# Kernel tuning notes

Hardware: AMD Instinct MI355X
Metric: run time of the kernel (lower is better)

Reference implementation:

```python
import jax, jax.numpy as jnp
import numpy as np
from jax import lax

B, T, U, V = 4, 200, 100, 1024
D_ENC, D_DEC, J = 144, 320, 320


def setup_inputs() -> dict:
    key = jax.random.key(0)
    ks = jax.random.split(key, 8)
    s = lambda d: 1.0 / np.sqrt(d).astype(np.float32)
    return {
        "enc_out": jax.random.normal(ks[0], (B, T, D_ENC), jnp.float32),
        "dec_out": jax.random.normal(ks[1], (B, U + 1, D_DEC), jnp.float32),
        "W_enc": jax.random.normal(ks[2], (D_ENC, J), jnp.float32) * s(D_ENC),
        "b_enc": jnp.zeros((J,), jnp.float32),
        "W_dec": jax.random.normal(ks[3], (D_DEC, J), jnp.float32) * s(D_DEC),
        "b_dec": jnp.zeros((J,), jnp.float32),
        "W_out": jax.random.normal(ks[4], (J, V), jnp.float32) * s(J),
        "b_out": jnp.zeros((V,), jnp.float32),
        "targets": jax.random.randint(ks[5], (B, U), 1, V, jnp.int32),
        "enc_lengths": jax.random.randint(ks[6], (B,), T // 2, T + 1, jnp.int32),
        "target_lengths": jax.random.randint(ks[7], (B,), U // 2, U + 1, jnp.int32),
    }


def _rnnt_loss(log_probs, targets, enc_lengths, target_lengths):
    # log_probs: [B, T, U+1, V]; blank index = 0 (matches RNNTLoss(blank=0))
    blank_lp = log_probs[..., 0]  # [B, T, U+1]
    idx = jnp.broadcast_to(targets[:, None, :, None].astype(jnp.int32), (B, T, U, 1))
    emit_lp = jnp.take_along_axis(log_probs[:, :, :U, :], idx, axis=-1)[..., 0]  # [B, T, U]

    # alpha[0, u] = sum of emit log-probs along u at t=0
    alpha0 = jnp.concatenate(
        [jnp.zeros((B, 1), log_probs.dtype), jnp.cumsum(emit_lp[:, 0, :], axis=1)], axis=1
    )  # [B, U+1]

    def row(a, emit_t):
        # a: alpha_prev + blank (vertical transitions), [B, U+1]; emit_t: [B, U]
        def step(prev, xs):
            a_u, e_prev = xs
            cur = jnp.logaddexp(a_u, prev + e_prev)
            return cur, cur
        _, rest = lax.scan(step, a[:, 0], (a[:, 1:].T, emit_t.T))  # rest: [U, B]
        return jnp.concatenate([a[:, :1], rest.T], axis=1)

    def t_step(alpha_prev, xs):
        blank_prev, emit_t = xs
        alpha_t = row(alpha_prev + blank_prev, emit_t)
        return alpha_t, alpha_t

    xs = (jnp.swapaxes(blank_lp[:, :-1, :], 0, 1), jnp.swapaxes(emit_lp[:, 1:, :], 0, 1))
    _, alphas_rest = lax.scan(t_step, alpha0, xs)  # [T-1, B, U+1]
    alphas = jnp.concatenate([alpha0[None], alphas_rest], axis=0)  # [T, B, U+1]

    b_idx = jnp.arange(B)
    t_idx = enc_lengths - 1
    ll = alphas[t_idx, b_idx, target_lengths] + blank_lp[b_idx, t_idx, target_lengths]
    return jnp.mean(-ll)  # reduction='mean' over batch


def reference(enc_out, dec_out, W_enc, b_enc, W_dec, b_dec, W_out, b_out, targets, enc_lengths, target_lengths):
    enc_p = enc_out @ W_enc + b_enc  # [B, T, J]
    dec_p = dec_out @ W_dec + b_dec  # [B, U+1, J]
    joint = jnp.tanh(enc_p[:, :, None, :] + dec_p[:, None, :, :])  # [B, T, U+1, J]
    logits = joint @ W_out + b_out  # [B, T, U+1, V]
    log_probs = jax.nn.log_softmax(logits, axis=-1)
    return _rnnt_loss(log_probs, targets, enc_lengths, target_lengths)
```

## Files before the change

kernel.cpp:

```cpp
#include <hip/hip_runtime.h>
#include <hip/hip_bf16.h>
#include <math.h>

#define B_ 4
#define T_ 200
#define U_ 100
#define V_ 1024
#define DE 144
#define DD 320
#define J_ 320
#define M_TOT (B_ * T_ * (U_ + 1))
#define SSTR 328
#define DSTR 104
#define NDIAG 300
#define LOG2E 1.4426950408889634f

typedef __attribute__((ext_vector_type(8))) short bf16x8_t;
typedef __attribute__((ext_vector_type(4))) float f32x4_t;

__device__ __forceinline__ float fast_tanh(float x) {
    float e = exp2f(x * (2.0f * LOG2E));
    float r = __frcp_rn(e + 1.0f);
    return fmaf(-2.0f, r, 1.0f);
}

__device__ __forceinline__ ushort f2bf(float x) {
    uint u = __float_as_uint(x);
    uint r = (u + 0x7FFFu + ((u >> 16) & 1u)) >> 16;
    return (ushort)r;
}

template <int K>
__device__ __forceinline__ void proj_body(const float* __restrict__ X,
                                          const float* __restrict__ W,
                                          const float* __restrict__ bias,
                                          float* __restrict__ Y,
                                          int r0, int R, float* sx, int tid) {
    constexpr int QK = K / 4;
    for (int q = tid; q < 16 * QK; q += 640) {
        int row = q / QK;
        int kq = q - row * QK;
        int r = r0 + row;
        if (r >= R) r = R - 1;
        *(float4*)&sx[row * K + kq * 4] = *(const float4*)&X[r * K + kq * 4];
    }
    __syncthreads();
    const int half = (tid >= 320) ? 1 : 0;
    const int c = tid - half * 320;
    float acc[8];
#pragma unroll
    for (int i = 0; i < 8; i++) acc[i] = 0.0f;
    for (int k = 0; k < K; k += 4) {
        float w0 = W[(k + 0) * 320 + c];
        float w1 = W[(k + 1) * 320 + c];
        float w2 = W[(k + 2) * 320 + c];
        float w3 = W[(k + 3) * 320 + c];
#pragma unroll
        for (int i = 0; i < 8; i++) {
            const float4 x4 = *(const float4*)&sx[(half * 8 + i) * K + k];
            acc[i] = fmaf(x4.x, w0, acc[i]);
            acc[i] = fmaf(x4.y, w1, acc[i]);
            acc[i] = fmaf(x4.z, w2, acc[i]);
            acc[i] = fmaf(x4.w, w3, acc[i]);
        }
    }
    const float bb = bias[c];
#pragma unroll
    for (int i = 0; i < 8; i++) {
        int r = r0 + half * 8 + i;
        if (r < R) Y[r * 320 + c] = acc[i] + bb;
    }
}

__global__ __launch_bounds__(640) void prep_kernel(
    const float* __restrict__ enc_out, const float* __restrict__ dec_out,
    const float* __restrict__ W_enc, const float* __restrict__ b_enc,
    const float* __restrict__ W_dec, const float* __restrict__ b_dec,
    const float* __restrict__ W_out,
    float* __restrict__ enc_p, float* __restrict__ dec_p,
    ushort* __restrict__ Wt) {
    __shared__ float sx[16 * 320];
    const int bid = blockIdx.x;
    const int tid = threadIdx.x;
    if (bid < 50) {
        proj_body<DE>(enc_out, W_enc, b_enc, enc_p, bid * 16, B_ * T_, sx, tid);
    } else if (bid < 76) {
        proj_body<DD>(dec_out, W_dec, b_dec, dec_p, (bid - 50) * 16,
                      B_ * (U_ + 1), sx, tid);
    } else {
        int idx = (bid - 76) * 640 + tid;
        int k = idx >> 10;
        int v = idx & 1023;
        ushort b = f2bf(W_out[idx]);
        int frag = (v >> 4) * 10 + (k >> 5);
        int lane = (v & 15) | (((k >> 3) & 3) << 4);
        int elem = k & 7;
        Wt[frag * 512 + lane * 8 + elem] = b;
    }
}

__global__ __launch_bounds__(1024, 4) void joint_mfma(
    const float* __restrict__ enc_p, const float* __restrict__ dec_p,
    const ushort* __restrict__ Wt, const float* __restrict__ b_out,
    const int* __restrict__ targets,
    float* __restrict__ bsk, float* __restrict__ esk) {
    __shared__ ushort sh[64 * SSTR];
    __shared__ float partm[16][64];
    __shared__ float parts[16][64];
    __shared__ float lse_sh[64];
    __shared__ int tgt_sh[64];

    const int tid = threadIdx.x;
    const int r0 = blockIdx.x * 64;

    if (tid < 64) {
        int rc = r0 + tid;
        int tg = -1;
        if (rc < M_TOT) {
            int b = rc / 20200;
            int rem = rc - b * 20200;
            int u = rem - (rem / 101) * 101;
            if (u < U_) tg = targets[b * U_ + u];
        }
        tgt_sh[tid] = tg;
    }

    {
        const int si = tid >> 4;
        const int sq = tid & 15;
        int rc = r0 + si;
        if (rc > M_TOT - 1) rc = M_TOT - 1;
        int b = rc / 20200;
        int rem = rc - b * 20200;
        int t = rem / 101;
        int u = rem - t * 101;
        const float4* ep = (const float4*)&enc_p[(b * 200 + t) * 320];
        const float4* dp = (const float4*)&dec_p[(b * 101 + u) * 320];
        ushort* shp = &sh[si * SSTR];
#pragma unroll
        for (int it = 0; it < 5; it++) {
            int kq = sq + it * 16;
            float4 e = ep[kq];
            float4 dd = dp[kq];
            float t0 = fast_tanh(e.x + dd.x);
            float t1 = fast_tanh(e.y + dd.y);
            float t2 = fast_tanh(e.z + dd.z);
            float t3 = fast_tanh(e.w + dd.w);
            __hip_bfloat162 p0 = __float22bfloat162_rn(make_float2(t0, t1));
            __hip_bfloat162 p1 = __float22bfloat162_rn(make_float2(t2, t3));
            uint2 pk;
            pk.x = *(uint*)&p0;
            pk.y = *(uint*)&p1;
            *(uint2*)&shp[kq * 4] = pk;
        }
    }
    __syncthreads();

    const int wave = tid >> 6;
    const int lane = tid & 63;
    const int lrow = lane & 15;
    const int lk = (lane >> 4) * 8;
    const int cb16 = wave * 4;

    f32x4_t acc[4][4];
#pragma unroll
    for (int mt = 0; mt < 4; mt++)
#pragma unroll
        for (int nt = 0; nt < 4; nt++) acc[mt][nt] = (f32x4_t)(0.0f);

    for (int ks = 0; ks < 10; ks++) {
        bf16x8_t a[4];
#pragma unroll
        for (int mt = 0; mt < 4; mt++)
            a[mt] = *(const bf16x8_t*)&sh[(mt * 16 + lrow) * SSTR + ks * 32 + lk];
#pragma unroll
        for (int nt = 0; nt < 4; nt++) {
            bf16x8_t bfr = *(const bf16x8_t*)&Wt[(((cb16 + nt) * 10 + ks) << 9) + lane * 8];
            __builtin_amdgcn_s_setprio(1);
#pragma unroll
            for (int mt = 0; mt < 4; mt++)
                acc[mt][nt] = __builtin_amdgcn_mfma_f32_16x16x32_bf16(a[mt], bfr, acc[mt][nt], 0, 0, 0);
            __builtin_amdgcn_s_setprio(0);
        }
    }

    float bo[4];
#pragma unroll
    for (int nt = 0; nt < 4; nt++) bo[nt] = b_out[wave * 64 + nt * 16 + lrow];
#pragma unroll
    for (int mt = 0; mt < 4; mt++)
#pragma unroll
        for (int nt = 0; nt < 4; nt++) acc[mt][nt] += bo[nt];

#pragma unroll
    for (int mt = 0; mt < 4; mt++) {
#pragma unroll
        for (int j = 0; j < 4; j++) {
            float m = fmaxf(fmaxf(acc[mt][0][j], acc[mt][1][j]),
                            fmaxf(acc[mt][2][j], acc[mt][3][j]));
#pragma unroll
            for (int off = 1; off < 16; off <<= 1)
                m = fmaxf(m, __shfl_xor(m, off, 16));
            float mm = m * LOG2E;
            float s = exp2f(fmaf(acc[mt][0][j], LOG2E, -mm));
            s += exp2f(fmaf(acc[mt][1][j], LOG2E, -mm));
            s += exp2f(fmaf(acc[mt][2][j], LOG2E, -mm));
            s += exp2f(fmaf(acc[mt][3][j], LOG2E, -mm));
#pragma unroll
            for (int off = 1; off < 16; off <<= 1)
                s += __shfl_xor(s, off, 16);
            if (lrow == 0) {
                int row = mt * 16 + (lane >> 4) * 4 + j;
                partm[wave][row] = m;
                parts[wave][row] = s;
            }
        }
    }
    __syncthreads();
    if (tid < 64) {
        float m = partm[0][tid];
        float s = parts[0][tid];
#pragma unroll
        for (int w = 1; w < 16; w++) {
            float mo = partm[w][tid], so = parts[w][tid];
            float M = fmaxf(m, mo);
            s = s * __expf(m - M) + so * __expf(mo - M);
            m = M;
        }
        lse_sh[tid] = m + __logf(s);
    }
    __syncthreads();

#pragma unroll
    for (int mt = 0; mt < 4; mt++) {
#pragma unroll
        for (int j = 0; j < 4; j++) {
            int lr = mt * 16 + (lane >> 4) * 4 + j;
            int r = r0 + lr;
            if (r >= M_TOT) continue;
            int tc = tgt_sh[lr];
            bool isblank = (wave == 0) && (lrow == 0);
            bool isemit = (tc >= 0) && ((tc >> 6) == wave) && ((tc & 15) == lrow);
            if (isblank || isemit) {
                int b = r / 20200;
                int rem = r - b * 20200;
                int t = rem / 101;
                int u = rem - t * 101;
                float lse = lse_sh[lr];
                if (isblank)
                    bsk[(b * NDIAG + t + u) * DSTR + u] = acc[mt][0][j] - lse;
                if (isemit) {
                    int ntl = (tc >> 4) & 3;
                    float v = acc[mt][0][j];
#pragma unroll
                    for (int nt = 1; nt < 4; nt++)
                        if (nt == ntl) v = acc[mt][nt][j];
                    esk[(b * NDIAG + t + u) * DSTR + u] = v - lse;
                }
            }
        }
    }
}

__global__ __launch_bounds__(256) void alpha8_kernel(
    const float* __restrict__ bsk, const float* __restrict__ esk,
    const int* __restrict__ enc_len, const int* __restrict__ tgt_len,
    float* __restrict__ out) {
    __shared__ float ll_sh[B_];
    const int tid = threadIdx.x;
    const int b = tid >> 6;
    const int l = tid & 63;
    const float* Bp = bsk + b * (NDIAG * DSTR);
    const float* Ep = esk + b * (NDIAG * DSTR);
    const int el = enc_len[b];
    const int tl = tgt_len[b];
    const int dfin = el - 1 + tl;

    float a1 = (l == 0) ? 0.0f : -INFINITY;
    float a2 = -INFINITY;

    float rb1[8], rb2[8], re1[8], re2[8];
#pragma unroll
    for (int k = 0; k < 8; k++) {
        rb1[k] = Bp[k * DSTR + l];
        rb2[k] = Bp[k * DSTR + 64 + l];
        re1[k] = Ep[k * DSTR + l];
        re2[k] = Ep[k * DSTR + 64 + l];
    }

    for (int dc = 1; dc <= 297; dc += 8) {
#pragma unroll
        for (int q = 0; q < 8; q++) {
            const int d = dc + q;
            if (d > NDIAG - 1) continue;
            const int sc = q;
            const int sm = (q + 1) & 7;
            float cb1 = rb1[sc], cb2 = rb2[sc], ce1 = re1[sc], ce2 = re2[sc];
            float mb1 = rb1[sm], mb2 = rb2[sm];
            int dn = d + 7;
            if (dn > NDIAG - 1) dn = NDIAG - 1;
            rb1[sc] = Bp[dn * DSTR + l];
            rb2[sc] = Bp[dn * DSTR + 64 + l];
            re1[sc] = Ep[dn * DSTR + l];
            re2[sc] = Ep[dn * DSTR + 64 + l];

            float pe1 = __shfl_up(ce1, 1, 64);
            float e1hi = __shfl(ce1, 63, 64);
            float pe2s = __shfl_up(ce2, 1, 64);
            float pe2 = (l == 0) ? e1hi : pe2s;
            float pa1 = __shfl_up(a1, 1, 64);
            float a1hi = __shfl(a1, 63, 64);
            float pa2s = __shfl_up(a2, 1, 64);
            float pa2 = (l == 0) ? a1hi : pa2s;

            const int t1 = d - l;
            float va = a1 + cb1;
            float vb = (l >= 1) ? pa1 + pe1 : -INFINITY;
            float M = fmaxf(va, vb);
            float v1 = (M == -INFINITY)
                           ? -INFINITY
                           : M + __logf(1.0f + __expf(fminf(va, vb) - M));
            if (t1 < 0 || t1 >= T_ || l > U_) v1 = -INFINITY;

            const int t2 = d - 64 - l;
            float va2 = a2 + cb2;
            float vb2 = pa2 + pe2;
            float M2 = fmaxf(va2, vb2);
            float v2 = (M2 == -INFINITY)
                           ? -INFINITY
                           : M2 + __logf(1.0f + __expf(fminf(va2, vb2) - M2));
            if (t2 < 0 || t2 >= T_ || (64 + l) > U_) v2 = -INFINITY;

            if (d == dfin) {
                if (l == tl) ll_sh[b] = v1 + mb1;
                if (64 + l == tl) ll_sh[b] = v2 + mb2;
            }
            a1 = v1;
            a2 = v2;
        }
    }
    __syncthreads();
    if (tid == 0)
        out[0] = -0.25f * (ll_sh[0] + ll_sh[1] + ll_sh[2] + ll_sh[3]);
}

extern "C" void kernel_launch(void* const* d_in, const int* in_sizes, int n_in,
                              void* d_out, int out_size, void* d_ws, size_t ws_size,
                              hipStream_t stream) {
    const float* enc_out = (const float*)d_in[0];
    const float* dec_out = (const float*)d_in[1];
    const float* W_enc = (const float*)d_in[2];
    const float* b_enc = (const float*)d_in[3];
    const float* W_dec = (const float*)d_in[4];
    const float* b_dec = (const float*)d_in[5];
    const float* W_out = (const float*)d_in[6];
    const float* b_out = (const float*)d_in[7];
    const int* targets = (const int*)d_in[8];
    const int* enc_len = (const int*)d_in[9];
    const int* tgt_len = (const int*)d_in[10];

    float* ws = (float*)d_ws;
    float* enc_p = ws;
    float* dec_p = enc_p + B_ * T_ * J_;
    float* bsk = dec_p + B_ * (U_ + 1) * J_;
    float* esk = bsk + B_ * NDIAG * DSTR;
    ushort* Wt = (ushort*)(esk + B_ * NDIAG * DSTR);

    prep_kernel<<<588, 640, 0, stream>>>(enc_out, dec_out, W_enc, b_enc,
                                         W_dec, b_dec, W_out, enc_p, dec_p, Wt);

    joint_mfma<<<(M_TOT + 63) / 64, 1024, 0, stream>>>(
        enc_p, dec_p, Wt, b_out, targets, bsk, esk);

    alpha8_kernel<<<1, 256, 0, stream>>>(bsk, esk, enc_len, tgt_len, (float*)d_out);
}
```

Measured before the change: 228.6 us.

## Split joint GEMM vocab across two 512-thread blocks with separate LSE combine kernel

Each 64-row tile is now handled by two 512-thread blocks, each covering half the vocabulary. Each block writes a partial max and sum-exp plus the raw blank and emit logits to scratch, and a new combine kernel merges the two halves into log-probs for the skewed alpha buffers. The intent is to use smaller blocks for better occupancy and scheduling, at the cost of computing tanh/joint activations twice per tile, an extra kernel launch, and extra global traffic. The alpha kernel's prefetch depth is also cut from 8 to 4 diagonals.

```diff
diff --git a/kernel.cpp b/kernel.cpp
--- a/kernel.cpp
+++ b/kernel.cpp
@@ -10,6 +10,7 @@
 #define DD 320
 #define J_ 320
 #define M_TOT (B_ * T_ * (U_ + 1))
+#define M_PAD 80832
 #define SSTR 328
 #define DSTR 104
 #define NDIAG 300
@@ -99,19 +100,22 @@
     }
 }
 
-__global__ __launch_bounds__(1024, 4) void joint_mfma(
+__global__ __launch_bounds__(512, 4) void joint_mfma(
     const float* __restrict__ enc_p, const float* __restrict__ dec_p,
     const ushort* __restrict__ Wt, const float* __restrict__ b_out,
     const int* __restrict__ targets,
-    float* __restrict__ bsk, float* __restrict__ esk) {
+    float* __restrict__ pm, float* __restrict__ ps,
+    float* __restrict__ pbl, float* __restrict__ pem) {
     __shared__ ushort sh[64 * SSTR];
-    __shared__ float partm[16][64];
-    __shared__ float parts[16][64];
-    __shared__ float lse_sh[64];
+    __shared__ float partm[8][64];
+    __shared__ float parts[8][64];
     __shared__ int tgt_sh[64];
 
     const int tid = threadIdx.x;
-    const int r0 = blockIdx.x * 64;
+    const int bid = blockIdx.x;
+    const int tile = bid >> 1;
+    const int hf = bid & 1;
+    const int r0 = tile * 64;
 
     if (tid < 64) {
         int rc = r0 + tid;
@@ -126,8 +130,8 @@
     }
 
     {
-        const int si = tid >> 4;
-        const int sq = tid & 15;
+        const int si = tid >> 3;
+        const int sq = tid & 7;
         int rc = r0 + si;
         if (rc > M_TOT - 1) rc = M_TOT - 1;
         int b = rc / 20200;
@@ -138,8 +142,8 @@
         const float4* dp = (const float4*)&dec_p[(b * 101 + u) * 320];
         ushort* shp = &sh[si * SSTR];
 #pragma unroll
-        for (int it = 0; it < 5; it++) {
-            int kq = sq + it * 16;
+        for (int it = 0; it < 10; it++) {
+            int kq = it * 8 + sq;
             float4 e = ep[kq];
             float4 dd = dp[kq];
             float t0 = fast_tanh(e.x + dd.x);
@@ -160,7 +164,7 @@
     const int lane = tid & 63;
     const int lrow = lane & 15;
     const int lk = (lane >> 4) * 8;
-    const int cb16 = wave * 4;
+    const int vt0 = hf * 32 + wave * 4;
 
     f32x4_t acc[4][4];
 #pragma unroll
@@ -175,7 +179,7 @@
             a[mt] = *(const bf16x8_t*)&sh[(mt * 16 + lrow) * SSTR + ks * 32 + lk];
 #pragma unroll
         for (int nt = 0; nt < 4; nt++) {
-            bf16x8_t bfr = *(const bf16x8_t*)&Wt[(((cb16 + nt) * 10 + ks) << 9) + lane * 8];
+            bf16x8_t bfr = *(const bf16x8_t*)&Wt[(((vt0 + nt) * 10 + ks) << 9) + lane * 8];
             __builtin_amdgcn_s_setprio(1);
 #pragma unroll
             for (int mt = 0; mt < 4; mt++)
@@ -186,7 +190,8 @@
 
     float bo[4];
 #pragma unroll
-    for (int nt = 0; nt < 4; nt++) bo[nt] = b_out[wave * 64 + nt * 16 + lrow];
+    for (int nt = 0; nt < 4; nt++)
+        bo[nt] = b_out[hf * 512 + wave * 64 + nt * 16 + lrow];
 #pragma unroll
     for (int mt = 0; mt < 4; mt++)
 #pragma unroll
@@ -221,15 +226,18 @@
         float m = partm[0][tid];
         float s = parts[0][tid];
 #pragma unroll
-        for (int w = 1; w < 16; w++) {
+        for (int w = 1; w < 8; w++) {
             float mo = partm[w][tid], so = parts[w][tid];
             float M = fmaxf(m, mo);
             s = s * __expf(m - M) + so * __expf(mo - M);
             m = M;
         }
-        lse_sh[tid] = m + __logf(s);
-    }
-    __syncthreads();
+        int r = r0 + tid;
+        if (r < M_TOT) {
+            pm[r * 2 + hf] = m;
+            ps[r * 2 + hf] = s;
+        }
+    }
 
 #pragma unroll
     for (int mt = 0; mt < 4; mt++) {
@@ -239,30 +247,43 @@
             int r = r0 + lr;
             if (r >= M_TOT) continue;
             int tc = tgt_sh[lr];
-            bool isblank = (wave == 0) && (lrow == 0);
-            bool isemit = (tc >= 0) && ((tc >> 6) == wave) && ((tc & 15) == lrow);
-            if (isblank || isemit) {
-                int b = r / 20200;
-                int rem = r - b * 20200;
-                int t = rem / 101;
-                int u = rem - t * 101;
-                float lse = lse_sh[lr];
-                if (isblank)
-                    bsk[(b * NDIAG + t + u) * DSTR + u] = acc[mt][0][j] - lse;
-                if (isemit) {
-                    int ntl = (tc >> 4) & 3;
-                    float v = acc[mt][0][j];
-#pragma unroll
-                    for (int nt = 1; nt < 4; nt++)
-                        if (nt == ntl) v = acc[mt][nt][j];
-                    esk[(b * NDIAG + t + u) * DSTR + u] = v - lse;
-                }
+            bool isblank = (hf == 0) && (wave == 0) && (lrow == 0);
+            bool isemit = (tc >= 0) && ((tc >> 9) == hf) &&
+                          (((tc >> 6) & 7) == wave) && ((tc & 15) == lrow);
+            if (isblank) pbl[r] = acc[mt][0][j];
+            if (isemit) {
+                int ntl = (tc >> 4) & 3;
+                float v = acc[mt][0][j];
+#pragma unroll
+                for (int nt = 1; nt < 4; nt++)
+                    if (nt == ntl) v = acc[mt][nt][j];
+                pem[r] = v;
             }
         }
     }
 }
 
-__global__ __launch_bounds__(256) void alpha8_kernel(
+__global__ __launch_bounds__(256) void combine_kernel(
+    const float* __restrict__ pm, const float* __restrict__ ps,
+    const float* __restrict__ pbl, const float* __restrict__ pem,
+    float* __restrict__ bsk, float* __restrict__ esk) {
+    int r = blockIdx.x * 256 + threadIdx.x;
+    if (r >= M_TOT) return;
+    float m0 = pm[r * 2], m1 = pm[r * 2 + 1];
+    float s0 = ps[r * 2], s1 = ps[r * 2 + 1];
+    float m = fmaxf(m0, m1);
+    float s = s0 * __expf(m0 - m) + s1 * __expf(m1 - m);
+    float lse = m + __logf(s);
+    int b = r / 20200;
+    int rem = r - b * 20200;
+    int t = rem / 101;
+    int u = rem - t * 101;
+    int base = (b * NDIAG + t + u) * DSTR + u;
+    bsk[base] = pbl[r] - lse;
+    if (u < U_) esk[base] = pem[r] - lse;
+}
+
+__global__ __launch_bounds__(256, 1) void alpha4_kernel(
     const float* __restrict__ bsk, const float* __restrict__ esk,
     const int* __restrict__ enc_len, const int* __restrict__ tgt_len,
     float* __restrict__ out) {
@@ -279,25 +300,25 @@
     float a1 = (l == 0) ? 0.0f : -INFINITY;
     float a2 = -INFINITY;
 
-    float rb1[8], rb2[8], re1[8], re2[8];
-#pragma unroll
-    for (int k = 0; k < 8; k++) {
+    float rb1[4], rb2[4], re1[4], re2[4];
+#pragma unroll
+    for (int k = 0; k < 4; k++) {
         rb1[k] = Bp[k * DSTR + l];
         rb2[k] = Bp[k * DSTR + 64 + l];
         re1[k] = Ep[k * DSTR + l];
         re2[k] = Ep[k * DSTR + 64 + l];
     }
 
-    for (int dc = 1; dc <= 297; dc += 8) {
-#pragma unroll
-        for (int q = 0; q < 8; q++) {
+    for (int dc = 1; dc <= 297; dc += 4) {
+#pragma unroll
+        for (int q = 0; q < 4; q++) {
             const int d = dc + q;
             if (d > NDIAG - 1) continue;
             const int sc = q;
-            const int sm = (q + 1) & 7;
+            const int sm = (q + 1) & 3;
             float cb1 = rb1[sc], cb2 = rb2[sc], ce1 = re1[sc], ce2 = re2[sc];
             float mb1 = rb1[sm], mb2 = rb2[sm];
-            int dn = d + 7;
+            int dn = d + 3;
             if (dn > NDIAG - 1) dn = NDIAG - 1;
             rb1[sc] = Bp[dn * DSTR + l];
             rb2[sc] = Bp[dn * DSTR + 64 + l];
@@ -364,13 +385,20 @@
     float* dec_p = enc_p + B_ * T_ * J_;
     float* bsk = dec_p + B_ * (U_ + 1) * J_;
     float* esk = bsk + B_ * NDIAG * DSTR;
-    ushort* Wt = (ushort*)(esk + B_ * NDIAG * DSTR);
+    float* pm = esk + B_ * NDIAG * DSTR;
+    float* ps = pm + 2 * M_PAD;
+    float* pbl = ps + 2 * M_PAD;
+    float* pem = pbl + M_PAD;
+    ushort* Wt = (ushort*)(pem + M_PAD);
 
     prep_kernel<<<588, 640, 0, stream>>>(enc_out, dec_out, W_enc, b_enc,
                                          W_dec, b_dec, W_out, enc_p, dec_p, Wt);
 
-    joint_mfma<<<(M_TOT + 63) / 64, 1024, 0, stream>>>(
-        enc_p, dec_p, Wt, b_out, targets, bsk, esk);
-
-    alpha8_kernel<<<1, 256, 0, stream>>>(bsk, esk, enc_len, tgt_len, (float*)d_out);
-}
+    joint_mfma<<<(M_PAD / 64) * 2, 512, 0, stream>>>(
+        enc_p, dec_p, Wt, b_out, targets, pm, ps, pbl, pem);
+
+    combine_kernel<<<(M_TOT + 255) / 256, 256, 0, stream>>>(pm, ps, pbl, pem,
+                                                            bsk, esk);
+
+    alpha4_kernel<<<1, 256, 0, stream>>>(bsk, esk, enc_len, tgt_len, (float*)d_out);
+}
```

After: 235.9 us. 3.2% more time.
